# Optimization experiments

Measured on AMD Instinct MI355X. Metric: run time of the kernel, lower is better.

Reference implementation:

```python
import jax, jax.numpy as jnp
import numpy as np

D_QUERY = 512
D_AUDIO = 512
D_OUT = 512
B, HW, S = 16, 4096, 1024


def setup_inputs() -> dict:
    key = jax.random.key(0)
    ks = jax.random.split(key, 8)
    sc_q = 1.0 / np.sqrt(D_QUERY)
    sc_a = 1.0 / np.sqrt(D_AUDIO)
    return {
        "x": jax.random.normal(ks[0], (B, HW, D_QUERY), dtype=jnp.float32),
        "audio_embed": jax.random.normal(ks[1], (B, S, D_AUDIO), dtype=jnp.float32),
        "Wq": jax.random.uniform(ks[2], (D_QUERY, D_OUT), jnp.float32, -sc_q, sc_q),
        "bq": jax.random.uniform(ks[3], (D_OUT,), jnp.float32, -sc_q, sc_q),
        "Wk": jax.random.uniform(ks[4], (D_AUDIO, D_OUT), jnp.float32, -sc_a, sc_a),
        "bk": jax.random.uniform(ks[5], (D_OUT,), jnp.float32, -sc_a, sc_a),
        "Wv": jax.random.uniform(ks[6], (D_AUDIO, D_OUT), jnp.float32, -sc_a, sc_a),
        "bv": jax.random.uniform(ks[7], (D_OUT,), jnp.float32, -sc_a, sc_a),
    }


def reference(x, audio_embed, Wq, bq, Wk, bk, Wv, bv):
    # Linear projections (nn.Linear: y = x @ W^T + b; we store W already transposed)
    Q = x @ Wq + bq                      # [B, HW, D_OUT]
    K = audio_embed @ Wk + bk            # [B, S, D_OUT]
    V = audio_embed @ Wv + bv            # [B, S, D_OUT]
    scale = 1.0 / (K.shape[-1] ** 0.5)   # divide by sqrt(d_out), per source
    scores = jnp.einsum("bnd,bsd->bns", Q, K) * scale  # [B, HW, S]
    attn = jax.nn.softmax(scores, axis=-1)
    return jnp.einsum("bns,bsd->bnd", attn, V)         # [B, HW, D_OUT]
```

## Files before the change

### kernel.cpp

```cpp
#include <hip/hip_runtime.h>
#include <hip/hip_bf16.h>

typedef __attribute__((ext_vector_type(8))) short bf16x8;
typedef __attribute__((ext_vector_type(4))) float f32x4;
typedef __attribute__((ext_vector_type(4))) unsigned short ushort4v;

#define AS1 __attribute__((address_space(1)))
#define AS3 __attribute__((address_space(3)))

__device__ __forceinline__ float bf_bits_to_f(short s) {
  unsigned int u = ((unsigned int)(unsigned short)s) << 16;
  union { unsigned int u; float f; } c; c.u = u; return c.f;
}
__device__ __forceinline__ unsigned short f_to_bf_bits(float f) {
  union { float f; unsigned int u; } c; c.f = f;
  unsigned int r = c.u + 0x7FFFu + ((c.u >> 16) & 1u);
  return (unsigned short)(r >> 16);
}

__device__ __forceinline__ int fsw(int row) { return ((row >> 1) & 3) << 4; }

__global__ __launch_bounds__(256) void cvt_bf16_kernel(const float* __restrict__ in,
                                                       unsigned short* __restrict__ out,
                                                       long n) {
  const long nchunks = n >> 2;
  const long stride = (long)gridDim.x * 256;
  for (long c = (long)blockIdx.x * 256 + threadIdx.x; c < nchunks; c += stride) {
    f32x4 v = *(const f32x4*)(in + c * 4);
    ushort4v o;
    o[0] = f_to_bf_bits(v[0]); o[1] = f_to_bf_bits(v[1]);
    o[2] = f_to_bf_bits(v[2]); o[3] = f_to_bf_bits(v[3]);
    *(ushort4v*)(out + c * 4) = o;
  }
}

__global__ __launch_bounds__(256) void transpose1_kernel(
    const float* __restrict__ W, unsigned short* __restrict__ T) {
  __shared__ float t[32][33];
  const int tx = threadIdx.x & 31, ty = threadIdx.x >> 5;
  const int n0 = blockIdx.x * 32, k0 = blockIdx.y * 32;
#pragma unroll
  for (int j = 0; j < 4; ++j)
    t[ty + 8 * j][tx] = W[(long)(k0 + ty + 8 * j) * 512 + n0 + tx];
  __syncthreads();
#pragma unroll
  for (int j = 0; j < 4; ++j)
    T[(long)(n0 + ty + 8 * j) * 512 + k0 + tx] = f_to_bf_bits(t[tx][ty + 8 * j]);
}

__global__ __launch_bounds__(256) void wvec_kernel(const float* __restrict__ Wk,
                                                   const float* __restrict__ bq,
                                                   float* __restrict__ w, const float s) {
  const int q = blockIdx.x * 4 + (threadIdx.x >> 6);
  const int lane = threadIdx.x & 63;
  const float* row = Wk + (long)q * 512 + lane * 8;
  const f32x4 a0 = *(const f32x4*)row;
  const f32x4 a1 = *(const f32x4*)(row + 4);
  const f32x4 b0 = *(const f32x4*)(bq + lane * 8);
  const f32x4 b1 = *(const f32x4*)(bq + lane * 8 + 4);
  float d = a0[0]*b0[0] + a0[1]*b0[1] + a0[2]*b0[2] + a0[3]*b0[3]
          + a1[0]*b1[0] + a1[1]*b1[1] + a1[2]*b1[2] + a1[3]*b1[3];
  for (int off = 1; off < 64; off <<= 1) d += __shfl_xor(d, off);
  if (lane == 0) w[q] = d * s;
}

__global__ __launch_bounds__(256) void cvec_kernel(const unsigned short* __restrict__ ab,
                                                   const float* __restrict__ w,
                                                   float* __restrict__ cv) {
  const long row = (long)blockIdx.x * 4 + (threadIdx.x >> 6);
  const int lane = threadIdx.x & 63;
  const bf16x8 a = *(const bf16x8*)(ab + row * 512 + lane * 8);
  const f32x4 w0 = *(const f32x4*)(w + lane * 8);
  const f32x4 w1 = *(const f32x4*)(w + lane * 8 + 4);
  float d = 0.f;
#pragma unroll
  for (int e = 0; e < 4; ++e) d += bf_bits_to_f(a[e]) * w0[e];
#pragma unroll
  for (int e = 0; e < 4; ++e) d += bf_bits_to_f(a[4 + e]) * w1[e];
  for (int off = 1; off < 64; off <<= 1) d += __shfl_xor(d, off);
  if (lane == 0) cv[row] = d;
}

template <bool BIAS, bool TRANSOUT, bool AFP32>
__global__ __launch_bounds__(256) void gemm_kernel(
    const void* __restrict__ Aptr,
    const unsigned short* __restrict__ BT,
    const float* __restrict__ bias,
    unsigned short* __restrict__ Cout,
    const int K, const float scale,
    const long strideA, const long strideBT, const long strideC, const int ldc,
    const int nx, const int ny) {
  __shared__ unsigned short lds[8192];
  const int nwg = gridDim.x;
  const int chunk = nwg >> 3;
  const int bid = blockIdx.x;
  const int swz = (bid & 7) * chunk + (bid >> 3);
  const int bx = swz % nx;
  const int t1 = swz / nx;
  const int by = t1 % ny;
  const int bz = t1 / ny;

  const int tid = threadIdx.x;
  const int lane = tid & 63;
  const int wv = tid >> 6;
  const int wr = wv >> 1, wc = wv & 1;
  const unsigned short* Ab = (const unsigned short*)Aptr + (long)bz * strideA + (long)by * 128 * K;
  const float* Af = (const float*)Aptr + (long)bz * strideA + (long)by * 128 * K;
  const unsigned short* Bb = BT + (long)bz * strideBT + (long)bx * 128 * K;

  f32x4 acc[4][4];
#pragma unroll
  for (int m = 0; m < 4; ++m)
#pragma unroll
    for (int n = 0; n < 4; ++n) acc[m][n] = (f32x4){0.f, 0.f, 0.f, 0.f};

  const int r15 = lane & 15, g = lane >> 4;
  const int kiters = K >> 5;
  const int asw = fsw(r15);

  int arow[2], acs[2];
#pragma unroll
  for (int i = 0; i < 2; ++i) {
    const int c = i * 4 + wv;
    const int boff = c * 1024 + lane * 16;
    arow[i] = boff >> 6;
    acs[i] = (boff & 63) ^ fsw(arow[i]);
  }
  f32x4 pa[2][2];
  if (AFP32) {
#pragma unroll
    for (int i = 0; i < 2; ++i) {
      const float* s = Af + (long)arow[i] * K + (acs[i] >> 1);
      pa[i][0] = *(const f32x4*)s;
      pa[i][1] = *(const f32x4*)(s + 4);
    }
  }

  for (int kt = 0; kt < kiters; ++kt) {
#pragma unroll
    for (int i = 0; i < 2; ++i) {
      const int c = i * 4 + wv;
      const char* srcB = (const char*)Bb + (long)arow[i] * (K * 2) + kt * 64 + acs[i];
      __builtin_amdgcn_global_load_lds(
          (const AS1 void*)srcB, (AS3 void*)(lds + 4096 + c * 512), 16, 0, 0);
      if (!AFP32) {
        const char* srcA = (const char*)Ab + (long)arow[i] * (K * 2) + kt * 64 + acs[i];
        __builtin_amdgcn_global_load_lds(
            (const AS1 void*)srcA, (AS3 void*)(lds + c * 512), 16, 0, 0);
      }
    }
    if (AFP32) {
#pragma unroll
      for (int i = 0; i < 2; ++i) {
        const int c = i * 4 + wv;
        bf16x8 w;
#pragma unroll
        for (int e = 0; e < 4; ++e) {
          w[e] = (short)f_to_bf_bits(pa[i][0][e]);
          w[4 + e] = (short)f_to_bf_bits(pa[i][1][e]);
        }
        *(bf16x8*)&lds[c * 512 + lane * 8] = w;
      }
      if (kt < kiters - 1) {
#pragma unroll
        for (int i = 0; i < 2; ++i) {
          const float* s = Af + (long)arow[i] * K + (kt + 1) * 32 + (acs[i] >> 1);
          pa[i][0] = *(const f32x4*)s;
          pa[i][1] = *(const f32x4*)(s + 4);
        }
      }
    }
    __syncthreads();

    bf16x8 af[4], bf[4];
#pragma unroll
    for (int m = 0; m < 4; ++m)
      af[m] = *(const bf16x8*)((const char*)lds + (wr * 64 + m * 16 + r15) * 64 + (g * 16 ^ asw));
#pragma unroll
    for (int n = 0; n < 4; ++n)
      bf[n] = *(const bf16x8*)((const char*)lds + 8192 +
                               (wc * 64 + n * 16 + r15) * 64 + (g * 16 ^ asw));
#pragma unroll
    for (int m = 0; m < 4; ++m)
#pragma unroll
      for (int n = 0; n < 4; ++n)
        acc[m][n] = __builtin_amdgcn_mfma_f32_16x16x32_bf16(af[m], bf[n], acc[m][n], 0, 0, 0);
    __syncthreads();
  }

  const long crow0 = (long)by * 128 + wr * 64;
  const long ccol0 = (long)bx * 128 + wc * 64;
#pragma unroll
  for (int n = 0; n < 4; ++n) {
    const long col = ccol0 + n * 16 + r15;
    const float bv = BIAS ? bias[col] : 0.f;
#pragma unroll
    for (int m = 0; m < 4; ++m) {
      const f32x4 v = acc[m][n];
#pragma unroll
      for (int j = 0; j < 4; ++j) {
        const long row = crow0 + m * 16 + g * 4 + j;
        const float val = (v[j] + bv) * scale;
        const long idx = TRANSOUT ? (col * (long)ldc + row) : (row * (long)ldc + col);
        (Cout + (long)bz * strideC)[idx] = f_to_bf_bits(val);
      }
    }
  }
}

template <bool EXPSTATS, bool DIVSTATS>
__global__ __launch_bounds__(1024) void gemm256_kernel(
    const unsigned short* __restrict__ A,
    const unsigned short* __restrict__ BT,
    void* __restrict__ Cout,
    const int K,
    const long strideA, const long strideBT, const long strideC, const int ldc,
    const int nx, const int ny, float* __restrict__ stats,
    const float* __restrict__ cbias) {
  __shared__ __align__(16) char halfb[4][32768];
  __shared__ float ssum[256][4];
  __shared__ float invl[256];

  const int nwg = gridDim.x;
  const int chunk = nwg >> 3;
  const int bid = blockIdx.x;
  const int swz = (bid & 7) * chunk + (bid >> 3);
  const int bx = swz % nx;
  const int t1 = swz / nx;
  const int by = t1 % ny;
  const int bz = t1 / ny;

  const int tid = threadIdx.x;
  const int lane = tid & 63;
  const int w = tid >> 6;
  const int wm = w >> 2, wn = w & 3;
  const int r15 = lane & 15, g = lane >> 4;
  const int asw = fsw(r15);

  const char* Abyt = (const char*)(A + (long)bz * strideA + (long)by * 256 * K);
  const char* Bbyt = (const char*)(BT + (long)bz * strideBT + (long)bx * 256 * K);
  const long rsb = (long)K * 2;

  if (DIVSTATS) {
    if (tid < 256) {
      const f32x4 s = *(const f32x4*)&stats[((long)bz * 4096 + (long)by * 256 + tid) * 4];
      invl[tid] = 1.f / (s[0] + s[1] + s[2] + s[3]);
    }
  }
  __builtin_amdgcn_sched_barrier(0);

  const int srow = tid >> 2;
  const int scol = ((tid & 3) << 4) ^ fsw(srow);
  const long aoff = (long)srow * rsb + scol;
  const int dbase = tid * 16;

  auto stage = [&](int s) {
    char* h = halfb[s & 3];
    const long kb = (long)s * 64;
    __builtin_amdgcn_global_load_lds((const AS1 void*)(Abyt + aoff + kb),
                                     (AS3 void*)(h + dbase), 16, 0, 0);
    __builtin_amdgcn_global_load_lds((const AS1 void*)(Bbyt + aoff + kb),
                                     (AS3 void*)(h + 16384 + dbase), 16, 0, 0);
  };

  f32x4 acc[4][4];
#pragma unroll
  for (int m = 0; m < 4; ++m)
#pragma unroll
    for (int n = 0; n < 4; ++n) acc[m][n] = (f32x4){0.f, 0.f, 0.f, 0.f};

  const int kslices = K >> 5;

  stage(0);
  stage(1);
  stage(2);
  asm volatile("s_waitcnt vmcnt(4)" ::: "memory");
  __builtin_amdgcn_s_barrier();
  __builtin_amdgcn_sched_barrier(0);

  for (int s = 0; s < kslices; ++s) {
    const char* hA = halfb[s & 3];
    const char* hB = halfb[s & 3] + 16384;
    bf16x8 fa[4], fb[4];
#pragma unroll
    for (int m = 0; m < 4; ++m)
      fa[m] = *(const bf16x8*)(hA + (wm * 64 + m * 16 + r15) * 64 + ((g * 16) ^ asw));
#pragma unroll
    for (int n = 0; n < 4; ++n)
      fb[n] = *(const bf16x8*)(hB + (wn * 64 + n * 16 + r15) * 64 + ((g * 16) ^ asw));
    __builtin_amdgcn_sched_barrier(0);
    if (s < kslices - 2) asm volatile("s_waitcnt vmcnt(2)" ::: "memory");
    else                 asm volatile("s_waitcnt vmcnt(0)" ::: "memory");
    __builtin_amdgcn_s_barrier();
    asm volatile("s_waitcnt lgkmcnt(0)" ::: "memory");
    __builtin_amdgcn_sched_barrier(0);
    if (s + 3 < kslices) stage(s + 3);
    __builtin_amdgcn_s_setprio(1);
#pragma unroll
    for (int m = 0; m < 4; ++m)
#pragma unroll
      for (int n = 0; n < 4; ++n)
        acc[m][n] = __builtin_amdgcn_mfma_f32_16x16x32_bf16(fa[m], fb[n], acc[m][n], 0, 0, 0);
    __builtin_amdgcn_s_setprio(0);
    __builtin_amdgcn_sched_barrier(0);
  }

  if (EXPSTATS) {
    float cb[4];
#pragma unroll
    for (int n = 0; n < 4; ++n)
      cb[n] = cbias[(long)bz * 1024 + (long)bx * 256 + wn * 64 + n * 16 + r15];
#pragma unroll
    for (int m = 0; m < 4; ++m)
#pragma unroll
      for (int n = 0; n < 4; ++n)
#pragma unroll
        for (int j = 0; j < 4; ++j) acc[m][n][j] = __expf(acc[m][n][j] + cb[n]);
#pragma unroll
    for (int m = 0; m < 4; ++m)
#pragma unroll
      for (int j = 0; j < 4; ++j) {
        float s = acc[m][0][j] + acc[m][1][j] + acc[m][2][j] + acc[m][3][j];
        s += __shfl_xor(s, 1);
        s += __shfl_xor(s, 2);
        s += __shfl_xor(s, 4);
        s += __shfl_xor(s, 8);
        if (r15 == 0) ssum[wm * 64 + m * 16 + g * 4 + j][wn] = s;
      }
    __syncthreads();
    if (tid < 256) {
      const float t = ssum[tid][0] + ssum[tid][1] + ssum[tid][2] + ssum[tid][3];
      stats[((long)bz * 4096 + (long)by * 256 + tid) * 4 + bx] = t;
    }
  }

  const long crow0 = (long)by * 256 + wm * 64;
  const long ccol0 = (long)bx * 256 + wn * 64;
#pragma unroll
  for (int m = 0; m < 4; ++m)
#pragma unroll
    for (int j = 0; j < 4; ++j) {
      const int rl = wm * 64 + m * 16 + g * 4 + j;
      const long row = crow0 + m * 16 + g * 4 + j;
#pragma unroll
      for (int n = 0; n < 4; ++n) {
        const long col = ccol0 + n * 16 + r15;
        if (EXPSTATS) {
          ((unsigned short*)Cout + (long)bz * strideC)[row * (long)ldc + col] =
              f_to_bf_bits(acc[m][n][j]);
        } else {
          const float sc = DIVSTATS ? invl[rl] : 1.f;
          ((float*)Cout + (long)bz * strideC)[row * (long)ldc + col] = acc[m][n][j] * sc;
        }
      }
    }
}

extern "C" void kernel_launch(void* const* d_in, const int* in_sizes, int n_in,
                              void* d_out, int out_size, void* d_ws, size_t ws_size,
                              hipStream_t stream) {
  (void)in_sizes; (void)n_in; (void)out_size; (void)ws_size;
  const float* x     = (const float*)d_in[0];
  const float* audio = (const float*)d_in[1];
  const float* Wq    = (const float*)d_in[2];
  const float* bq    = (const float*)d_in[3];
  const float* Wk    = (const float*)d_in[4];
  const float* bk    = (const float*)d_in[5];  (void)bk;
  const float* Wv    = (const float*)d_in[6];
  const float* bv    = (const float*)d_in[7];
  float* out = (float*)d_out;

  const float s = 0.044194173824159216f;

  char* ws = (char*)d_ws;
  size_t off = 0;
  auto carve = [&](size_t bytes) { char* p = ws + off; off += (bytes + 255) & ~(size_t)255; return p; };
  unsigned short* xb  = (unsigned short*)carve((size_t)65536 * 512 * 2);
  unsigned short* ab  = (unsigned short*)carve((size_t)16384 * 512 * 2);
  unsigned short* wkb = (unsigned short*)carve((size_t)512 * 512 * 2);
  unsigned short* wvt = (unsigned short*)carve((size_t)512 * 512 * 2);
  unsigned short* G   = (unsigned short*)carve((size_t)512 * 512 * 2);
  unsigned short* KMb = (unsigned short*)carve((size_t)16384 * 512 * 2);
  unsigned short* Vt  = (unsigned short*)carve((size_t)16384 * 512 * 2);
  unsigned short* Pb  = (unsigned short*)carve((size_t)65536 * 1024 * 2);
  float*          ls  = (float*)carve((size_t)65536 * 4 * 4);
  float*          wv_ = (float*)carve((size_t)512 * 4);
  float*          cv  = (float*)carve((size_t)16384 * 4);

  cvt_bf16_kernel<<<2048, 256, 0, stream>>>(x, xb, (long)65536 * 512);
  cvt_bf16_kernel<<<1024, 256, 0, stream>>>(audio, ab, (long)16384 * 512);
  cvt_bf16_kernel<<<256, 256, 0, stream>>>(Wk, wkb, (long)512 * 512);
  transpose1_kernel<<<dim3(16, 16), 256, 0, stream>>>(Wv, wvt);
  gemm_kernel<false, false, true><<<16, 256, 0, stream>>>(
      Wq, wkb, nullptr, G, 512, s, 0, 0, 0, 512, 4, 4);
  wvec_kernel<<<128, 256, 0, stream>>>(Wk, bq, wv_, s);
  cvec_kernel<<<4096, 256, 0, stream>>>(ab, wv_, cv);
  gemm_kernel<true, true, false><<<4 * 8 * 16, 256, 0, stream>>>(
      ab, wvt, bv, Vt, 512, 1.f, (long)1024 * 512, 0, (long)512 * 1024, 1024, 4, 8);
  gemm_kernel<false, false, false><<<4 * 8 * 16, 256, 0, stream>>>(
      ab, G, nullptr, KMb, 512, 1.f, (long)1024 * 512, 0, (long)1024 * 512, 512, 4, 8);
  gemm256_kernel<true, false><<<4 * 16 * 16, 1024, 0, stream>>>(
      xb, KMb, Pb, 512,
      (long)4096 * 512, (long)1024 * 512, (long)4096 * 1024, 1024, 4, 16, ls, cv);
  gemm256_kernel<false, true><<<2 * 16 * 16, 1024, 0, stream>>>(
      Pb, Vt, out, 1024,
      (long)4096 * 1024, (long)512 * 1024, (long)4096 * 512, 512, 2, 16, ls, nullptr);
}
```

Baseline: 328.4 us.

## Shrink attention GEMM tiles to 256x128 single-buffer and drop audio bf16 copy

The two big attention GEMMs move from 1024-thread 256x256 tiles with a 4-stage async LDS pipeline to 512-thread 256x128 tiles with one 24KB buffer and plain syncthreads. The aim is to fit several workgroups per CU (launch_bounds 512,4) and get more blocks in flight. The softmax row statistics grow to 8 partials per row. Separately, the audio bf16 conversion pass is removed: the K/V projection GEMMs and the cvec dot product now read fp32 audio directly. The price is that the explicit prefetch overlap is lost, and A tiles are reloaded twice as often across the N dimension.

```diff
diff --git a/kernel.cpp b/kernel.cpp
--- a/kernel.cpp
+++ b/kernel.cpp
@@ -32,20 +32,6 @@
     o[2] = f_to_bf_bits(v[2]); o[3] = f_to_bf_bits(v[3]);
     *(ushort4v*)(out + c * 4) = o;
   }
-}
-
-__global__ __launch_bounds__(256) void transpose1_kernel(
-    const float* __restrict__ W, unsigned short* __restrict__ T) {
-  __shared__ float t[32][33];
-  const int tx = threadIdx.x & 31, ty = threadIdx.x >> 5;
-  const int n0 = blockIdx.x * 32, k0 = blockIdx.y * 32;
-#pragma unroll
-  for (int j = 0; j < 4; ++j)
-    t[ty + 8 * j][tx] = W[(long)(k0 + ty + 8 * j) * 512 + n0 + tx];
-  __syncthreads();
-#pragma unroll
-  for (int j = 0; j < 4; ++j)
-    T[(long)(n0 + ty + 8 * j) * 512 + k0 + tx] = f_to_bf_bits(t[tx][ty + 8 * j]);
 }
 
 __global__ __launch_bounds__(256) void wvec_kernel(const float* __restrict__ Wk,
@@ -64,19 +50,17 @@
   if (lane == 0) w[q] = d * s;
 }
 
-__global__ __launch_bounds__(256) void cvec_kernel(const unsigned short* __restrict__ ab,
+__global__ __launch_bounds__(256) void cvec_kernel(const float* __restrict__ audio,
                                                    const float* __restrict__ w,
                                                    float* __restrict__ cv) {
   const long row = (long)blockIdx.x * 4 + (threadIdx.x >> 6);
   const int lane = threadIdx.x & 63;
-  const bf16x8 a = *(const bf16x8*)(ab + row * 512 + lane * 8);
+  const f32x4 a0 = *(const f32x4*)(audio + row * 512 + lane * 8);
+  const f32x4 a1 = *(const f32x4*)(audio + row * 512 + lane * 8 + 4);
   const f32x4 w0 = *(const f32x4*)(w + lane * 8);
   const f32x4 w1 = *(const f32x4*)(w + lane * 8 + 4);
-  float d = 0.f;
-#pragma unroll
-  for (int e = 0; e < 4; ++e) d += bf_bits_to_f(a[e]) * w0[e];
-#pragma unroll
-  for (int e = 0; e < 4; ++e) d += bf_bits_to_f(a[4 + e]) * w1[e];
+  float d = a0[0]*w0[0] + a0[1]*w0[1] + a0[2]*w0[2] + a0[3]*w0[3]
+          + a1[0]*w1[0] + a1[1]*w1[1] + a1[2]*w1[2] + a1[3]*w1[3];
   for (int off = 1; off < 64; off <<= 1) d += __shfl_xor(d, off);
   if (lane == 0) cv[row] = d;
 }
@@ -209,7 +193,7 @@
 }
 
 template <bool EXPSTATS, bool DIVSTATS>
-__global__ __launch_bounds__(1024) void gemm256_kernel(
+__global__ __launch_bounds__(512, 4) void gemm_mn_kernel(
     const unsigned short* __restrict__ A,
     const unsigned short* __restrict__ BT,
     void* __restrict__ Cout,
@@ -217,8 +201,8 @@
     const long strideA, const long strideBT, const long strideC, const int ldc,
     const int nx, const int ny, float* __restrict__ stats,
     const float* __restrict__ cbias) {
-  __shared__ __align__(16) char halfb[4][32768];
-  __shared__ float ssum[256][4];
+  __shared__ __align__(16) char buf[24576];
+  __shared__ float ssum[256][2];
   __shared__ float invl[256];
 
   const int nwg = gridDim.x;
@@ -233,68 +217,54 @@
   const int tid = threadIdx.x;
   const int lane = tid & 63;
   const int w = tid >> 6;
-  const int wm = w >> 2, wn = w & 3;
+  const int wm = w >> 1, wn = w & 1;
   const int r15 = lane & 15, g = lane >> 4;
   const int asw = fsw(r15);
 
   const char* Abyt = (const char*)(A + (long)bz * strideA + (long)by * 256 * K);
-  const char* Bbyt = (const char*)(BT + (long)bz * strideBT + (long)bx * 256 * K);
+  const char* Bbyt = (const char*)(BT + (long)bz * strideBT + (long)bx * 128 * K);
   const long rsb = (long)K * 2;
 
   if (DIVSTATS) {
     if (tid < 256) {
-      const f32x4 s = *(const f32x4*)&stats[((long)bz * 4096 + (long)by * 256 + tid) * 4];
-      invl[tid] = 1.f / (s[0] + s[1] + s[2] + s[3]);
-    }
-  }
-  __builtin_amdgcn_sched_barrier(0);
+      const float* sp = stats + ((long)bz * 4096 + (long)by * 256 + tid) * 8;
+      const f32x4 s0 = *(const f32x4*)sp;
+      const f32x4 s1 = *(const f32x4*)(sp + 4);
+      invl[tid] = 1.f / (s0[0] + s0[1] + s0[2] + s0[3] + s1[0] + s1[1] + s1[2] + s1[3]);
+    }
+  }
 
   const int srow = tid >> 2;
   const int scol = ((tid & 3) << 4) ^ fsw(srow);
-  const long aoff = (long)srow * rsb + scol;
+  const long aoff0 = (long)srow * rsb + scol;
+  const long aoff1 = (long)(srow + 128) * rsb + scol;
   const int dbase = tid * 16;
 
-  auto stage = [&](int s) {
-    char* h = halfb[s & 3];
+  f32x4 acc[4][4];
+#pragma unroll
+  for (int m = 0; m < 4; ++m)
+#pragma unroll
+    for (int n = 0; n < 4; ++n) acc[m][n] = (f32x4){0.f, 0.f, 0.f, 0.f};
+
+  const int kslices = K >> 5;
+
+  for (int s = 0; s < kslices; ++s) {
     const long kb = (long)s * 64;
-    __builtin_amdgcn_global_load_lds((const AS1 void*)(Abyt + aoff + kb),
-                                     (AS3 void*)(h + dbase), 16, 0, 0);
-    __builtin_amdgcn_global_load_lds((const AS1 void*)(Bbyt + aoff + kb),
-                                     (AS3 void*)(h + 16384 + dbase), 16, 0, 0);
-  };
-
-  f32x4 acc[4][4];
-#pragma unroll
-  for (int m = 0; m < 4; ++m)
-#pragma unroll
-    for (int n = 0; n < 4; ++n) acc[m][n] = (f32x4){0.f, 0.f, 0.f, 0.f};
-
-  const int kslices = K >> 5;
-
-  stage(0);
-  stage(1);
-  stage(2);
-  asm volatile("s_waitcnt vmcnt(4)" ::: "memory");
-  __builtin_amdgcn_s_barrier();
-  __builtin_amdgcn_sched_barrier(0);
-
-  for (int s = 0; s < kslices; ++s) {
-    const char* hA = halfb[s & 3];
-    const char* hB = halfb[s & 3] + 16384;
+    __builtin_amdgcn_global_load_lds((const AS1 void*)(Abyt + aoff0 + kb),
+                                     (AS3 void*)(buf + dbase), 16, 0, 0);
+    __builtin_amdgcn_global_load_lds((const AS1 void*)(Abyt + aoff1 + kb),
+                                     (AS3 void*)(buf + 8192 + dbase), 16, 0, 0);
+    __builtin_amdgcn_global_load_lds((const AS1 void*)(Bbyt + aoff0 + kb),
+                                     (AS3 void*)(buf + 16384 + dbase), 16, 0, 0);
+    __syncthreads();
+
     bf16x8 fa[4], fb[4];
 #pragma unroll
     for (int m = 0; m < 4; ++m)
-      fa[m] = *(const bf16x8*)(hA + (wm * 64 + m * 16 + r15) * 64 + ((g * 16) ^ asw));
+      fa[m] = *(const bf16x8*)(buf + (wm * 64 + m * 16 + r15) * 64 + ((g * 16) ^ asw));
 #pragma unroll
     for (int n = 0; n < 4; ++n)
-      fb[n] = *(const bf16x8*)(hB + (wn * 64 + n * 16 + r15) * 64 + ((g * 16) ^ asw));
-    __builtin_amdgcn_sched_barrier(0);
-    if (s < kslices - 2) asm volatile("s_waitcnt vmcnt(2)" ::: "memory");
-    else                 asm volatile("s_waitcnt vmcnt(0)" ::: "memory");
-    __builtin_amdgcn_s_barrier();
-    asm volatile("s_waitcnt lgkmcnt(0)" ::: "memory");
-    __builtin_amdgcn_sched_barrier(0);
-    if (s + 3 < kslices) stage(s + 3);
+      fb[n] = *(const bf16x8*)(buf + 16384 + (wn * 64 + n * 16 + r15) * 64 + ((g * 16) ^ asw));
     __builtin_amdgcn_s_setprio(1);
 #pragma unroll
     for (int m = 0; m < 4; ++m)
@@ -302,14 +272,14 @@
       for (int n = 0; n < 4; ++n)
         acc[m][n] = __builtin_amdgcn_mfma_f32_16x16x32_bf16(fa[m], fb[n], acc[m][n], 0, 0, 0);
     __builtin_amdgcn_s_setprio(0);
-    __builtin_amdgcn_sched_barrier(0);
+    __syncthreads();
   }
 
   if (EXPSTATS) {
     float cb[4];
 #pragma unroll
     for (int n = 0; n < 4; ++n)
-      cb[n] = cbias[(long)bz * 1024 + (long)bx * 256 + wn * 64 + n * 16 + r15];
+      cb[n] = cbias[(long)bz * 1024 + (long)bx * 128 + wn * 64 + n * 16 + r15];
 #pragma unroll
     for (int m = 0; m < 4; ++m)
 #pragma unroll
@@ -328,14 +298,12 @@
         if (r15 == 0) ssum[wm * 64 + m * 16 + g * 4 + j][wn] = s;
       }
     __syncthreads();
-    if (tid < 256) {
-      const float t = ssum[tid][0] + ssum[tid][1] + ssum[tid][2] + ssum[tid][3];
-      stats[((long)bz * 4096 + (long)by * 256 + tid) * 4 + bx] = t;
-    }
+    if (tid < 256)
+      stats[((long)bz * 4096 + (long)by * 256 + tid) * 8 + bx] = ssum[tid][0] + ssum[tid][1];
   }
 
   const long crow0 = (long)by * 256 + wm * 64;
-  const long ccol0 = (long)bx * 256 + wn * 64;
+  const long ccol0 = (long)bx * 128 + wn * 64;
 #pragma unroll
   for (int m = 0; m < 4; ++m)
 #pragma unroll
@@ -376,33 +344,48 @@
   size_t off = 0;
   auto carve = [&](size_t bytes) { char* p = ws + off; off += (bytes + 255) & ~(size_t)255; return p; };
   unsigned short* xb  = (unsigned short*)carve((size_t)65536 * 512 * 2);
-  unsigned short* ab  = (unsigned short*)carve((size_t)16384 * 512 * 2);
   unsigned short* wkb = (unsigned short*)carve((size_t)512 * 512 * 2);
   unsigned short* wvt = (unsigned short*)carve((size_t)512 * 512 * 2);
   unsigned short* G   = (unsigned short*)carve((size_t)512 * 512 * 2);
   unsigned short* KMb = (unsigned short*)carve((size_t)16384 * 512 * 2);
   unsigned short* Vt  = (unsigned short*)carve((size_t)16384 * 512 * 2);
   unsigned short* Pb  = (unsigned short*)carve((size_t)65536 * 1024 * 2);
-  float*          ls  = (float*)carve((size_t)65536 * 4 * 4);
+  float*          ls  = (float*)carve((size_t)65536 * 8 * 4);
   float*          wv_ = (float*)carve((size_t)512 * 4);
   float*          cv  = (float*)carve((size_t)16384 * 4);
 
   cvt_bf16_kernel<<<2048, 256, 0, stream>>>(x, xb, (long)65536 * 512);
-  cvt_bf16_kernel<<<1024, 256, 0, stream>>>(audio, ab, (long)16384 * 512);
   cvt_bf16_kernel<<<256, 256, 0, stream>>>(Wk, wkb, (long)512 * 512);
+  {
+  }
+  extern __global__ void transpose1_kernel(const float*, unsigned short*);
   transpose1_kernel<<<dim3(16, 16), 256, 0, stream>>>(Wv, wvt);
   gemm_kernel<false, false, true><<<16, 256, 0, stream>>>(
       Wq, wkb, nullptr, G, 512, s, 0, 0, 0, 512, 4, 4);
   wvec_kernel<<<128, 256, 0, stream>>>(Wk, bq, wv_, s);
-  cvec_kernel<<<4096, 256, 0, stream>>>(ab, wv_, cv);
-  gemm_kernel<true, true, false><<<4 * 8 * 16, 256, 0, stream>>>(
-      ab, wvt, bv, Vt, 512, 1.f, (long)1024 * 512, 0, (long)512 * 1024, 1024, 4, 8);
-  gemm_kernel<false, false, false><<<4 * 8 * 16, 256, 0, stream>>>(
-      ab, G, nullptr, KMb, 512, 1.f, (long)1024 * 512, 0, (long)1024 * 512, 512, 4, 8);
-  gemm256_kernel<true, false><<<4 * 16 * 16, 1024, 0, stream>>>(
+  cvec_kernel<<<4096, 256, 0, stream>>>(audio, wv_, cv);
+  gemm_kernel<true, true, true><<<4 * 8 * 16, 256, 0, stream>>>(
+      audio, wvt, bv, Vt, 512, 1.f, (long)1024 * 512, 0, (long)512 * 1024, 1024, 4, 8);
+  gemm_kernel<false, false, true><<<4 * 8 * 16, 256, 0, stream>>>(
+      audio, G, nullptr, KMb, 512, 1.f, (long)1024 * 512, 0, (long)1024 * 512, 512, 4, 8);
+  gemm_mn_kernel<true, false><<<8 * 16 * 16, 512, 0, stream>>>(
       xb, KMb, Pb, 512,
-      (long)4096 * 512, (long)1024 * 512, (long)4096 * 1024, 1024, 4, 16, ls, cv);
-  gemm256_kernel<false, true><<<2 * 16 * 16, 1024, 0, stream>>>(
+      (long)4096 * 512, (long)1024 * 512, (long)4096 * 1024, 1024, 8, 16, ls, cv);
+  gemm_mn_kernel<false, true><<<4 * 16 * 16, 512, 0, stream>>>(
       Pb, Vt, out, 1024,
-      (long)4096 * 1024, (long)512 * 1024, (long)4096 * 512, 512, 2, 16, ls, nullptr);
-}
+      (long)4096 * 1024, (long)512 * 1024, (long)4096 * 512, 512, 4, 16, ls, nullptr);
+}
+
+__global__ __launch_bounds__(256) void transpose1_kernel(
+    const float* __restrict__ W, unsigned short* __restrict__ T) {
+  __shared__ float t[32][33];
+  const int tx = threadIdx.x & 31, ty = threadIdx.x >> 5;
+  const int n0 = blockIdx.x * 32, k0 = blockIdx.y * 32;
+#pragma unroll
+  for (int j = 0; j < 4; ++j)
+    t[ty + 8 * j][tx] = W[(long)(k0 + ty + 8 * j) * 512 + n0 + tx];
+  __syncthreads();
+#pragma unroll
+  for (int j = 0; j < 4; ++j)
+    T[(long)(n0 + ty + 8 * j) * 512 + k0 + tx] = f_to_bf_bits(t[tx][ty + 8 * j]);
+}
```

New measurement: 338.4 us. 3.0% more time.
